# Optimization experiments

Measured on AMD Instinct MI355X. Metric: run time of the kernel, lower is better.

Reference implementation:

```python
import jax, jax.numpy as jnp
import numpy as np

B, C_IN, H, W = 4, 128, 32, 128   # W must equal out_channels (fc_out acts on last dim)
C_OUT, NUM_HEADS = 128, 2
BN_EPS = 1e-5


def setup_inputs() -> dict:
    key = jax.random.key(0)
    ks = jax.random.split(key, 14)
    s = 0.05  # small init scale for weights
    d = {
        "x": jax.random.normal(ks[0], (B, C_IN, H, W), jnp.float32),
        "wq": jax.random.normal(ks[1], (C_OUT, C_IN), jnp.float32) * s,
        "bq": jax.random.normal(ks[2], (C_OUT,), jnp.float32) * s,
        "wk": jax.random.normal(ks[3], (C_OUT, C_IN), jnp.float32) * s,
        "bk": jax.random.normal(ks[4], (C_OUT,), jnp.float32) * s,
        "wv": jax.random.normal(ks[5], (C_OUT, C_IN), jnp.float32) * s,
        "bv": jax.random.normal(ks[6], (C_OUT,), jnp.float32) * s,
        "fc_w": jax.random.normal(ks[7], (C_OUT, C_OUT), jnp.float32) * s,
        "fc_b": jax.random.normal(ks[8], (C_OUT,), jnp.float32) * s,
        "bn_gamma": jnp.ones((C_OUT,), jnp.float32),
        "bn_beta": jnp.zeros((C_OUT,), jnp.float32),
        "bn_mean": jax.random.normal(ks[9], (C_OUT,), jnp.float32) * 0.1,
        "bn_var": jax.random.uniform(ks[10], (C_OUT,), jnp.float32, 0.5, 1.5),
        "prelu_a": jnp.full((1,), 0.25, jnp.float32),
    }
    return d


def reference(x, wq, bq, wk, bk, wv, bv, fc_w, fc_b,
              bn_gamma, bn_beta, bn_mean, bn_var, prelu_a):
    b, c_in, h, w = x.shape
    c_out = wq.shape[0]
    nh = NUM_HEADS
    dk = c_out // nh
    L = h * w
    xf = x.reshape(b, c_in, L)                                # (B, Cin, L)
    # 1x1 convs == per-token linear projections
    q = jnp.einsum('oi,bil->bol', wq, xf) + bq[:, None]       # (B, Cout, L)
    k = jnp.einsum('oi,bil->bol', wk, xf) + bk[:, None]
    v = jnp.einsum('oi,bil->bol', wv, xf) + bv[:, None]
    Q = q.reshape(b, nh, dk, L)                               # (B, h, d_k, L)
    K = k.reshape(b, nh, dk, L)
    V = v.reshape(b, nh, dk, L)
    # scaled dot-product attention over the L = H*W tokens
    scores = jnp.einsum('bhdl,bhdm->bhlm', Q, K) / jnp.sqrt(jnp.float32(dk))
    attn = jax.nn.softmax(scores, axis=-1)                    # (B, h, L, L)
    out = jnp.einsum('bhlm,bhdm->bhdl', attn, V)              # (B, h, d_k, L)
    out = out.reshape(b, c_out, h, w)                         # (B, Cout, H, W)
    # fc_out: torch Linear on the LAST dim (W == Cout)
    y = jnp.einsum('bchw,ow->bcho', out, fc_w) + fc_b         # (B, Cout, H, W)
    # BatchNorm2d (eval mode: running stats) over channel dim
    inv = jax.lax.rsqrt(bn_var + BN_EPS)
    y = (y - bn_mean[None, :, None, None]) * (inv * bn_gamma)[None, :, None, None] \
        + bn_beta[None, :, None, None]
    # PReLU (single shared slope); dropout is identity in eval
    y = jnp.where(y > 0, y, prelu_a[0] * y)
    return y
```

## Files before the change

kernel.cpp:

```cpp
#include <hip/hip_runtime.h>

typedef _Float16 f16x8 __attribute__((ext_vector_type(8)));
typedef _Float16 f16x4t __attribute__((ext_vector_type(4)));
typedef __fp16 h16x2 __attribute__((ext_vector_type(2)));
typedef float f32x4 __attribute__((ext_vector_type(4)));
typedef float f32x16 __attribute__((ext_vector_type(16)));
typedef unsigned int uint2v __attribute__((ext_vector_type(2)));

#define L_SZ 4096

__device__ __forceinline__ unsigned short f2h(float f) {
    _Float16 h = (_Float16)f;
    return __builtin_bit_cast(unsigned short, h);
}
__device__ __forceinline__ unsigned int pk2(float a, float b) {
    h16x2 p = __builtin_amdgcn_cvt_pkrtz(a, b);
    return __builtin_bit_cast(unsigned int, p);
}

#define SLOT(row, ci) ((((ci) * 64) + ((row) & 32) + (((row) & 31) ^ (ci))) * 8)

__global__ __launch_bounds__(256) void prep_kernel(
    const float* __restrict__ wq, const float* __restrict__ wk,
    const float* __restrict__ wv, const float* __restrict__ fcw,
    unsigned short* __restrict__ Wimg, unsigned short* __restrict__ Fimg)
{
    int e2 = blockIdx.x * 256 + threadIdx.x;
    if (e2 < 24576) {
        const float* src = (e2 < 8192) ? wq : (e2 < 16384 ? wk : wv);
        float2 v = *(const float2*)&src[(e2 * 2) & 16383];
        int e = e2 * 2;
        int o = e >> 7, ci = (e & 127) >> 3, j = e & 7;
        *(unsigned int*)&Wimg[o * 128 + ((ci ^ (o & 15)) * 8) + j] = pk2(v.x, v.y);
    } else {
        int fe = (e2 - 24576) * 2;
        float2 v = *(const float2*)&fcw[fe];
        int o = fe >> 7, ci = (fe & 127) >> 3, j = fe & 7;
        *(unsigned int*)&Fimg[o * 128 + ((ci ^ (o & 15)) * 8) + j] = pk2(v.x, v.y);
    }
}

__global__ __launch_bounds__(256, 1) void qkv_kernel(
    const float* __restrict__ x,
    const unsigned short* __restrict__ Wimg,
    const float* __restrict__ bq, const float* __restrict__ bk,
    const float* __restrict__ bv,
    unsigned short* __restrict__ Qp, unsigned short* __restrict__ Kp,
    unsigned short* __restrict__ Vp)
{
    int blk = blockIdx.x;
    int bidx = blk >> 6;
    int l0 = (blk & 63) * 64;
    int tid = threadIdx.x;
    int wave = tid >> 6, lane = tid & 63;
    int c = lane & 15, qd = lane >> 4;

    __shared__ __align__(16) unsigned short Ws[384 * 128];
    __shared__ __align__(16) unsigned short Sc[9216];

    #pragma unroll
    for (int t = 0; t < 24; ++t) {
        int i8 = (tid + t * 256) * 8;
        *(uint4*)&Ws[i8] = *(const uint4*)&Wimg[i8];
    }

    unsigned short* Xs = Sc;
    #pragma unroll
    for (int it = 0; it < 8; ++it) {
        int i  = (tid >> 4) + 16 * it;
        int l4 = (tid & 15) * 4;
        const float4 v = *(const float4*)&x[(bidx * 128 + i) * L_SZ + l0 + l4];
        float vv[4] = {v.x, v.y, v.z, v.w};
        int ci = i >> 3;
        #pragma unroll
        for (int u = 0; u < 4; ++u) {
            int l = l4 + u;
            Xs[l * 128 + ((ci ^ (l & 15)) * 8) + (i & 7)] = f2h(vv[u]);
        }
    }
    __syncthreads();

    f16x8 afrag[4];
    #pragma unroll
    for (int kc = 0; kc < 4; ++kc) {
        int l = wave * 16 + c;
        int ci = kc * 4 + qd;
        afrag[kc] = *(const f16x8*)&Xs[l * 128 + ((ci ^ (l & 15)) * 8)];
    }
    __syncthreads();

    f32x4 acc[24];
    #pragma unroll
    for (int nt = 0; nt < 24; ++nt) acc[nt] = (f32x4){0.f, 0.f, 0.f, 0.f};

    #pragma unroll
    for (int kc = 0; kc < 4; ++kc) {
        #pragma unroll
        for (int nt = 0; nt < 24; ++nt) {
            int o = nt * 16 + c;
            f16x8 bfrag = *(const f16x8*)&Ws[o * 128 + (((kc * 4 + qd) ^ c) * 8)];
            acc[nt] = __builtin_amdgcn_mfma_f32_16x16x32_f16(afrag[kc], bfrag, acc[nt], 0, 0, 0);
        }
    }

    unsigned short* Vt = Sc;
    const float s_q = 0.18033688011f;
    #pragma unroll
    for (int nt = 0; nt < 24; ++nt) {
        int p = nt >> 3;
        int o = (nt & 7) * 16 + c;
        int h = o >> 6, d = o & 63;
        #pragma unroll
        for (int r = 0; r < 4; ++r) {
            int ll = wave * 16 + qd * 4 + r;
            int l = l0 + ll;
            float val = acc[nt][r];
            if (p == 0) {
                val = (val + bq[o]) * s_q;
                Qp[((bidx * 2 + h) * L_SZ + l) * 64 + d] = f2h(val);
            } else if (p == 1) {
                val += bk[o];
                Kp[((bidx * 2 + h) * L_SZ + l) * 64 + d] = f2h(val);
            } else {
                val += bv[o];
                Vt[o * 72 + ll] = f2h(val);
            }
        }
    }
    __syncthreads();
    #pragma unroll
    for (int t = 0; t < 2; ++t) {
        int u = tid + t * 256;
        int row = u >> 2;
        int lc = (u & 3) * 16;
        uint4 a0 = *(const uint4*)&Vt[row * 72 + lc];
        uint4 a1 = *(const uint4*)&Vt[row * 72 + lc + 8];
        *(uint4*)&Vp[(size_t)(bidx * 128 + row) * L_SZ + l0 + lc] = a0;
        *(uint4*)&Vp[(size_t)(bidx * 128 + row) * L_SZ + l0 + lc + 8] = a1;
    }
}

__global__ __launch_bounds__(256, 4) void attn_kernel(
    const unsigned short* __restrict__ Qp, const unsigned short* __restrict__ Kp,
    const unsigned short* __restrict__ Vp,
    unsigned short* __restrict__ Opart, float* __restrict__ Mpart, float* __restrict__ Lpart)
{
    int raw = blockIdx.x;
    int blk = (raw & 7) * 128 + (raw >> 3);
    int lt = blk & 31;
    int bh = (blk >> 5) & 7;
    int sp = blk >> 8;
    int l0 = lt * 128;
    int tid = threadIdx.x;
    int wave = tid >> 6, lane = tid & 63;
    int ln = lane & 31, hi = lane >> 5;
    int b = bh >> 1, h = bh & 1;

    __shared__ __align__(16) unsigned short Ks[2][4096];
    __shared__ __align__(16) unsigned short Vs[2][4096];

    const unsigned short* Qb = Qp + (size_t)bh * L_SZ * 64;
    const unsigned short* Kb = Kp + (size_t)bh * L_SZ * 64;
    const unsigned short* Vb = Vp + ((size_t)b * 128 + h * 64) * L_SZ;

    int lq = l0 + wave * 32 + ln;
    f16x8 qf[4];
    #pragma unroll
    for (int kc = 0; kc < 4; ++kc)
        qf[kc] = *(const f16x8*)&Qb[(size_t)lq * 64 + kc * 16 + hi * 8];

    float m_st = -1e30f, lsum = 0.f;
    f32x16 acc0 = {}, acc1 = {};

    int urow = tid >> 3, uci = tid & 7;
    int mglob = sp * 1024;

    uint4 kreg[2], vreg[2];
    #pragma unroll
    for (int j = 0; j < 2; ++j) {
        int row = urow + j * 32;
        kreg[j] = *(const uint4*)&Kb[(size_t)(mglob + row) * 64 + uci * 8];
        vreg[j] = *(const uint4*)&Vb[(size_t)row * L_SZ + mglob + uci * 8];
    }
    #pragma unroll
    for (int j = 0; j < 2; ++j) {
        int row = urow + j * 32;
        *(uint4*)&Ks[0][SLOT(row, uci)] = kreg[j];
        *(uint4*)&Vs[0][SLOT(row, uci)] = vreg[j];
    }

    for (int it = 0; it < 16; ++it) {
        int cur = it & 1;
        __syncthreads();
        if (it < 15) {
            int m0 = mglob + (it + 1) * 64;
            #pragma unroll
            for (int j = 0; j < 2; ++j) {
                int row = urow + j * 32;
                kreg[j] = *(const uint4*)&Kb[(size_t)(m0 + row) * 64 + uci * 8];
                vreg[j] = *(const uint4*)&Vb[(size_t)row * L_SZ + m0 + uci * 8];
            }
        }

        __builtin_amdgcn_s_setprio(1);
        f32x16 s0 = {}, s1 = {};
        #pragma unroll
        for (int kc = 0; kc < 4; ++kc) {
            int cd = kc * 2 + hi;
            f16x8 k0 = *(const f16x8*)&Ks[cur][SLOT(ln, cd)];
            f16x8 k1 = *(const f16x8*)&Ks[cur][SLOT(32 + ln, cd)];
            s0 = __builtin_amdgcn_mfma_f32_32x32x16_f16(k0, qf[kc], s0, 0, 0, 0);
            s1 = __builtin_amdgcn_mfma_f32_32x32x16_f16(k1, qf[kc], s1, 0, 0, 0);
        }

        float t[8];
        #pragma unroll
        for (int r = 0; r < 8; ++r)
            t[r] = fmaxf(fmaxf(s0[r], s0[r + 8]), fmaxf(s1[r], s1[r + 8]));
        t[0] = fmaxf(t[0], t[4]); t[1] = fmaxf(t[1], t[5]);
        t[2] = fmaxf(t[2], t[6]); t[3] = fmaxf(t[3], t[7]);
        float mx = fmaxf(fmaxf(t[0], t[1]), fmaxf(t[2], t[3]));
        mx = fmaxf(mx, __shfl_xor(mx, 32));

        if (!__all(mx <= m_st + 8.0f)) {
            float mnew = fmaxf(m_st, mx);
            float alpha = exp2f(m_st - mnew);
            m_st = mnew;
            lsum *= alpha;
            #pragma unroll
            for (int r = 0; r < 16; ++r) { acc0[r] *= alpha; acc1[r] *= alpha; }
        }
        float rsum = 0.f;
        #pragma unroll
        for (int r = 0; r < 16; ++r) { float p = exp2f(s0[r] - m_st); s0[r] = p; rsum += p; }
        #pragma unroll
        for (int r = 0; r < 16; ++r) { float p = exp2f(s1[r] - m_st); s1[r] = p; rsum += p; }
        lsum += rsum;

        #pragma unroll
        for (int kc = 0; kc < 4; ++kc) {
            unsigned int a0, a1, a2, a3;
            if (kc == 0) {
                a0 = pk2(s0[0], s0[1]);  a1 = pk2(s0[2], s0[3]);
                a2 = pk2(s0[4], s0[5]);  a3 = pk2(s0[6], s0[7]);
            } else if (kc == 1) {
                a0 = pk2(s0[8], s0[9]);  a1 = pk2(s0[10], s0[11]);
                a2 = pk2(s0[12], s0[13]); a3 = pk2(s0[14], s0[15]);
            } else if (kc == 2) {
                a0 = pk2(s1[0], s1[1]);  a1 = pk2(s1[2], s1[3]);
                a2 = pk2(s1[4], s1[5]);  a3 = pk2(s1[6], s1[7]);
            } else {
                a0 = pk2(s1[8], s1[9]);  a1 = pk2(s1[10], s1[11]);
                a2 = pk2(s1[12], s1[13]); a3 = pk2(s1[14], s1[15]);
            }
            uint2v r02 = __builtin_amdgcn_permlane32_swap(a0, a2, false, false);
            uint2v r13 = __builtin_amdgcn_permlane32_swap(a1, a3, false, false);
            uint4 pw; pw.x = r02[0]; pw.y = r13[0]; pw.z = r02[1]; pw.w = r13[1];
            f16x8 pf = __builtin_bit_cast(f16x8, pw);
            int cd = kc * 2 + hi;
            f16x8 v0 = *(const f16x8*)&Vs[cur][SLOT(ln, cd)];
            f16x8 v1 = *(const f16x8*)&Vs[cur][SLOT(32 + ln, cd)];
            acc0 = __builtin_amdgcn_mfma_f32_32x32x16_f16(v0, pf, acc0, 0, 0, 0);
            acc1 = __builtin_amdgcn_mfma_f32_32x32x16_f16(v1, pf, acc1, 0, 0, 0);
        }
        __builtin_amdgcn_s_setprio(0);

        if (it < 15) {
            #pragma unroll
            for (int j = 0; j < 2; ++j) {
                int row = urow + j * 32;
                *(uint4*)&Ks[cur ^ 1][SLOT(row, uci)] = kreg[j];
                *(uint4*)&Vs[cur ^ 1][SLOT(row, uci)] = vreg[j];
            }
        }
    }

    float l_tot = lsum + __shfl_xor(lsum, 32);
    unsigned short* Ow = Opart + (size_t)(sp * 8 + bh) * 64 * 4096;
    #pragma unroll
    for (int r = 0; r < 16; ++r) {
        int d0 = (r & 3) + 8 * (r >> 2) + 4 * hi;
        Ow[(size_t)d0 * 4096 + lq] = f2h(acc0[r]);
        Ow[(size_t)(32 + d0) * 4096 + lq] = f2h(acc1[r]);
    }
    if (hi == 0) {
        Mpart[(sp * 8 + bh) * 4096 + lq] = m_st;
        Lpart[(sp * 8 + bh) * 4096 + lq] = l_tot;
    }
}

__global__ __launch_bounds__(256, 1) void fc_kernel(
    const unsigned short* __restrict__ Opart, const float* __restrict__ Mp,
    const float* __restrict__ Lp, const unsigned short* __restrict__ Fimg,
    const float* __restrict__ fc_b, const float* __restrict__ bn_g,
    const float* __restrict__ bn_b, const float* __restrict__ bn_m,
    const float* __restrict__ bn_v, const float* __restrict__ prelu_a,
    float* __restrict__ out)
{
    int raw = blockIdx.x;
    int blk = (raw & 7) * 32 + (raw >> 3);
    int r0 = blk * 64;
    int tid = threadIdx.x;
    int c0 = (r0 >> 5) & 127;
    int bh = (r0 >> 12) * 2 + (c0 >> 6);

    int wave = tid >> 6, lane = tid & 63;
    int c = lane & 15, qd = lane >> 4;
    int rw = r0 + wave * 16;
    int row = rw + c;
    int ch = (row >> 5) & 127, hh = row & 31, d = ch & 63;

    __shared__ __align__(16) unsigned short Fw[128 * 128];
    __shared__ __align__(16) unsigned short SclU[4096 * 4];

    uint4 ovr[4][4];
    #pragma unroll
    for (int kc = 0; kc < 4; ++kc) {
        int w0 = kc * 32 + qd * 8;
        #pragma unroll
        for (int s = 0; s < 4; ++s)
            ovr[kc][s] = *(const uint4*)&Opart[(size_t)(s * 8 + bh) * 262144 + (size_t)d * 4096 + hh * 128 + w0];
    }

    #pragma unroll
    for (int t = 0; t < 16; ++t) {
        int l = tid + t * 256;
        float m0 = Mp[(0 * 8 + bh) * 4096 + l], m1 = Mp[(1 * 8 + bh) * 4096 + l];
        float m2 = Mp[(2 * 8 + bh) * 4096 + l], m3 = Mp[(3 * 8 + bh) * 4096 + l];
        float mx = fmaxf(fmaxf(m0, m1), fmaxf(m2, m3));
        float a0 = exp2f(m0 - mx), a1 = exp2f(m1 - mx);
        float a2 = exp2f(m2 - mx), a3 = exp2f(m3 - mx);
        float den = a0 * Lp[(0 * 8 + bh) * 4096 + l] + a1 * Lp[(1 * 8 + bh) * 4096 + l]
                  + a2 * Lp[(2 * 8 + bh) * 4096 + l] + a3 * Lp[(3 * 8 + bh) * 4096 + l];
        float inv = 1.0f / den;
        int hl = l >> 7, ww = l & 127;
        int slot = hl * 128 + ((ww + hl) & 127);
        uint2 sc;
        sc.x = pk2(a0 * inv, a1 * inv);
        sc.y = pk2(a2 * inv, a3 * inv);
        *(uint2*)&SclU[slot * 4] = sc;
    }
    #pragma unroll
    for (int t = 0; t < 8; ++t) {
        int i8 = (tid + t * 256) * 8;
        *(uint4*)&Fw[i8] = *(const uint4*)&Fimg[i8];
    }
    __syncthreads();

    f16x8 af[4];
    #pragma unroll
    for (int kc = 0; kc < 4; ++kc) {
        int w0 = kc * 32 + qd * 8;
        f16x8 ov0 = __builtin_bit_cast(f16x8, ovr[kc][0]);
        f16x8 ov1 = __builtin_bit_cast(f16x8, ovr[kc][1]);
        f16x8 ov2 = __builtin_bit_cast(f16x8, ovr[kc][2]);
        f16x8 ov3 = __builtin_bit_cast(f16x8, ovr[kc][3]);
        #pragma unroll
        for (int j = 0; j < 8; ++j) {
            int slot = hh * 128 + ((w0 + j + hh) & 127);
            f16x4t sc = *(const f16x4t*)&SclU[slot * 4];
            float v = (float)ov0[j] * (float)sc[0] + (float)ov1[j] * (float)sc[1]
                    + (float)ov2[j] * (float)sc[2] + (float)ov3[j] * (float)sc[3];
            af[kc][j] = (_Float16)v;
        }
    }

    f32x4 acc[8];
    #pragma unroll
    for (int nt = 0; nt < 8; ++nt) acc[nt] = (f32x4){0.f, 0.f, 0.f, 0.f};
    #pragma unroll
    for (int kc = 0; kc < 4; ++kc) {
        #pragma unroll
        for (int nt = 0; nt < 8; ++nt) {
            int o = nt * 16 + c;
            f16x8 bf = *(const f16x8*)&Fw[o * 128 + (((kc * 4 + qd) ^ c) * 8)];
            acc[nt] = __builtin_amdgcn_mfma_f32_16x16x32_f16(af[kc], bf, acc[nt], 0, 0, 0);
        }
    }

    float pa = prelu_a[0];
    #pragma unroll
    for (int r = 0; r < 4; ++r) {
        int orow = rw + qd * 4 + r;
        int chn = (orow >> 5) & 127;
        float g  = bn_g[chn] * rsqrtf(bn_v[chn] + 1e-5f);
        float mn = bn_m[chn], bt = bn_b[chn];
        #pragma unroll
        for (int nt = 0; nt < 8; ++nt) {
            int o = nt * 16 + c;
            float y = (acc[nt][r] + fc_b[o] - mn) * g + bt;
            y = y > 0.f ? y : pa * y;
            out[(size_t)orow * 128 + o] = y;
        }
    }
}

extern "C" void kernel_launch(void* const* d_in, const int* in_sizes, int n_in,
                              void* d_out, int out_size, void* d_ws, size_t ws_size,
                              hipStream_t stream) {
    const float* x     = (const float*)d_in[0];
    const float* wq    = (const float*)d_in[1];
    const float* bq    = (const float*)d_in[2];
    const float* wk    = (const float*)d_in[3];
    const float* bk    = (const float*)d_in[4];
    const float* wv    = (const float*)d_in[5];
    const float* bv    = (const float*)d_in[6];
    const float* fcw_f = (const float*)d_in[7];
    const float* fcb   = (const float*)d_in[8];
    const float* bn_g  = (const float*)d_in[9];
    const float* bn_b  = (const float*)d_in[10];
    const float* bn_m  = (const float*)d_in[11];
    const float* bn_v  = (const float*)d_in[12];
    const float* pa    = (const float*)d_in[13];
    float* out = (float*)d_out;

    unsigned short* Qp  = (unsigned short*)d_ws;
    unsigned short* Kp  = Qp + 8 * L_SZ * 64;
    unsigned short* Vp  = Kp + 8 * L_SZ * 64;
    unsigned short* Opart = Vp + 8 * L_SZ * 64;
    float* Mpart = (float*)(Opart + 4 * 8 * 64 * L_SZ);
    float* Lpart = Mpart + 4 * 8 * L_SZ;
    unsigned short* Wimg = (unsigned short*)(Lpart + 4 * 8 * L_SZ);
    unsigned short* Fimg = Wimg + 384 * 128;

    hipLaunchKernelGGL(prep_kernel, dim3(128),  dim3(256), 0, stream,
                       wq, wk, wv, fcw_f, Wimg, Fimg);
    hipLaunchKernelGGL(qkv_kernel,  dim3(256),  dim3(256), 0, stream,
                       x, Wimg, bq, bk, bv, Qp, Kp, Vp);
    hipLaunchKernelGGL(attn_kernel, dim3(1024), dim3(256), 0, stream,
                       Qp, Kp, Vp, Opart, Mpart, Lpart);
    hipLaunchKernelGGL(fc_kernel,   dim3(256),  dim3(256), 0, stream,
                       Opart, Mpart, Lpart, Fimg, fcb, bn_g, bn_b, bn_m, bn_v, pa, out);
}
```

Baseline: 172.7 us.

## Split QKV and FC kernels across more blocks and tune attention softmax inner loop

The QKV projection now launches one block per (tile, projection) triple with a 128x128 weight slice, which cuts shared memory and registers so more blocks fit per CU. The FC kernel halves its rows per block, splits output columns across waves and hoists the BN parameters since each block now covers one channel. The attention loop switches to pointer increments, partial unrolling, a restructured max reduction, split exp-sum accumulators and hardware exp2/rcp intrinsics. Together these aim to raise occupancy and instruction-level parallelism. The cost is that the x tile is reloaded three times, plus extra block launches.

```diff
diff --git a/kernel.cpp b/kernel.cpp
--- a/kernel.cpp
+++ b/kernel.cpp
@@ -16,6 +16,20 @@
 __device__ __forceinline__ unsigned int pk2(float a, float b) {
     h16x2 p = __builtin_amdgcn_cvt_pkrtz(a, b);
     return __builtin_bit_cast(unsigned int, p);
+}
+__device__ __forceinline__ float fexp2(float x) {
+#if __has_builtin(__builtin_amdgcn_exp2f)
+    return __builtin_amdgcn_exp2f(x);
+#else
+    return exp2f(x);
+#endif
+}
+__device__ __forceinline__ float frcp(float x) {
+#if __has_builtin(__builtin_amdgcn_rcpf)
+    return __builtin_amdgcn_rcpf(x);
+#else
+    return 1.0f / x;
+#endif
 }
 
 #define SLOT(row, ci) ((((ci) * 64) + ((row) & 32) + (((row) & 31) ^ (ci))) * 8)
@@ -40,7 +54,7 @@
     }
 }
 
-__global__ __launch_bounds__(256, 1) void qkv_kernel(
+__global__ __launch_bounds__(256, 3) void qkv_kernel(
     const float* __restrict__ x,
     const unsigned short* __restrict__ Wimg,
     const float* __restrict__ bq, const float* __restrict__ bk,
@@ -48,20 +62,24 @@
     unsigned short* __restrict__ Qp, unsigned short* __restrict__ Kp,
     unsigned short* __restrict__ Vp)
 {
-    int blk = blockIdx.x;
-    int bidx = blk >> 6;
-    int l0 = (blk & 63) * 64;
+    int raw = blockIdx.x;
+    int v = (raw & 7) * 96 + (raw >> 3);
+    int tile = v / 3;
+    int p = v - tile * 3;
+    int bidx = tile >> 6;
+    int l0 = (tile & 63) * 64;
     int tid = threadIdx.x;
     int wave = tid >> 6, lane = tid & 63;
     int c = lane & 15, qd = lane >> 4;
 
-    __shared__ __align__(16) unsigned short Ws[384 * 128];
+    __shared__ __align__(16) unsigned short Ws[128 * 128];
     __shared__ __align__(16) unsigned short Sc[9216];
 
-    #pragma unroll
-    for (int t = 0; t < 24; ++t) {
+    const unsigned short* wsrc = Wimg + p * 16384;
+    #pragma unroll
+    for (int t = 0; t < 8; ++t) {
         int i8 = (tid + t * 256) * 8;
-        *(uint4*)&Ws[i8] = *(const uint4*)&Wimg[i8];
+        *(uint4*)&Ws[i8] = *(const uint4*)&wsrc[i8];
     }
 
     unsigned short* Xs = Sc;
@@ -69,8 +87,8 @@
     for (int it = 0; it < 8; ++it) {
         int i  = (tid >> 4) + 16 * it;
         int l4 = (tid & 15) * 4;
-        const float4 v = *(const float4*)&x[(bidx * 128 + i) * L_SZ + l0 + l4];
-        float vv[4] = {v.x, v.y, v.z, v.w};
+        const float4 vx = *(const float4*)&x[(bidx * 128 + i) * L_SZ + l0 + l4];
+        float vv[4] = {vx.x, vx.y, vx.z, vx.w};
         int ci = i >> 3;
         #pragma unroll
         for (int u = 0; u < 4; ++u) {
@@ -89,54 +107,65 @@
     }
     __syncthreads();
 
-    f32x4 acc[24];
-    #pragma unroll
-    for (int nt = 0; nt < 24; ++nt) acc[nt] = (f32x4){0.f, 0.f, 0.f, 0.f};
+    f32x4 acc[8];
+    #pragma unroll
+    for (int nt = 0; nt < 8; ++nt) acc[nt] = (f32x4){0.f, 0.f, 0.f, 0.f};
 
     #pragma unroll
     for (int kc = 0; kc < 4; ++kc) {
         #pragma unroll
-        for (int nt = 0; nt < 24; ++nt) {
+        for (int nt = 0; nt < 8; ++nt) {
             int o = nt * 16 + c;
             f16x8 bfrag = *(const f16x8*)&Ws[o * 128 + (((kc * 4 + qd) ^ c) * 8)];
             acc[nt] = __builtin_amdgcn_mfma_f32_16x16x32_f16(afrag[kc], bfrag, acc[nt], 0, 0, 0);
         }
     }
 
-    unsigned short* Vt = Sc;
     const float s_q = 0.18033688011f;
-    #pragma unroll
-    for (int nt = 0; nt < 24; ++nt) {
-        int p = nt >> 3;
-        int o = (nt & 7) * 16 + c;
-        int h = o >> 6, d = o & 63;
-        #pragma unroll
-        for (int r = 0; r < 4; ++r) {
-            int ll = wave * 16 + qd * 4 + r;
-            int l = l0 + ll;
-            float val = acc[nt][r];
-            if (p == 0) {
-                val = (val + bq[o]) * s_q;
-                Qp[((bidx * 2 + h) * L_SZ + l) * 64 + d] = f2h(val);
-            } else if (p == 1) {
-                val += bk[o];
-                Kp[((bidx * 2 + h) * L_SZ + l) * 64 + d] = f2h(val);
-            } else {
-                val += bv[o];
-                Vt[o * 72 + ll] = f2h(val);
+    if (p == 0) {
+        #pragma unroll
+        for (int nt = 0; nt < 8; ++nt) {
+            int o = nt * 16 + c;
+            int h = o >> 6, d = o & 63;
+            #pragma unroll
+            for (int r = 0; r < 4; ++r) {
+                int l = l0 + wave * 16 + qd * 4 + r;
+                Qp[((bidx * 2 + h) * L_SZ + l) * 64 + d] = f2h((acc[nt][r] + bq[o]) * s_q);
             }
         }
-    }
-    __syncthreads();
-    #pragma unroll
-    for (int t = 0; t < 2; ++t) {
-        int u = tid + t * 256;
-        int row = u >> 2;
-        int lc = (u & 3) * 16;
-        uint4 a0 = *(const uint4*)&Vt[row * 72 + lc];
-        uint4 a1 = *(const uint4*)&Vt[row * 72 + lc + 8];
-        *(uint4*)&Vp[(size_t)(bidx * 128 + row) * L_SZ + l0 + lc] = a0;
-        *(uint4*)&Vp[(size_t)(bidx * 128 + row) * L_SZ + l0 + lc + 8] = a1;
+    } else if (p == 1) {
+        #pragma unroll
+        for (int nt = 0; nt < 8; ++nt) {
+            int o = nt * 16 + c;
+            int h = o >> 6, d = o & 63;
+            #pragma unroll
+            for (int r = 0; r < 4; ++r) {
+                int l = l0 + wave * 16 + qd * 4 + r;
+                Kp[((bidx * 2 + h) * L_SZ + l) * 64 + d] = f2h(acc[nt][r] + bk[o]);
+            }
+        }
+    } else {
+        unsigned short* Vt = Sc;
+        #pragma unroll
+        for (int nt = 0; nt < 8; ++nt) {
+            int o = nt * 16 + c;
+            #pragma unroll
+            for (int r = 0; r < 4; ++r) {
+                int ll = wave * 16 + qd * 4 + r;
+                Vt[o * 72 + ll] = f2h(acc[nt][r] + bv[o]);
+            }
+        }
+        __syncthreads();
+        #pragma unroll
+        for (int t = 0; t < 2; ++t) {
+            int u = tid + t * 256;
+            int row = u >> 2;
+            int lc = (u & 3) * 16;
+            uint4 a0 = *(const uint4*)&Vt[row * 72 + lc];
+            uint4 a1 = *(const uint4*)&Vt[row * 72 + lc + 8];
+            *(uint4*)&Vp[(size_t)(bidx * 128 + row) * L_SZ + l0 + lc] = a0;
+            *(uint4*)&Vp[(size_t)(bidx * 128 + row) * L_SZ + l0 + lc + 8] = a1;
+        }
     }
 }
 
@@ -175,13 +204,14 @@
     int urow = tid >> 3, uci = tid & 7;
     int mglob = sp * 1024;
 
+    const unsigned short* kptr = Kb + (size_t)(mglob + urow) * 64 + uci * 8;
+    const unsigned short* vptr = Vb + (size_t)urow * L_SZ + mglob + uci * 8;
+
     uint4 kreg[2], vreg[2];
-    #pragma unroll
-    for (int j = 0; j < 2; ++j) {
-        int row = urow + j * 32;
-        kreg[j] = *(const uint4*)&Kb[(size_t)(mglob + row) * 64 + uci * 8];
-        vreg[j] = *(const uint4*)&Vb[(size_t)row * L_SZ + mglob + uci * 8];
-    }
+    kreg[0] = *(const uint4*)(kptr);
+    kreg[1] = *(const uint4*)(kptr + 2048);
+    vreg[0] = *(const uint4*)(vptr);
+    vreg[1] = *(const uint4*)(vptr + 32 * L_SZ);
     #pragma unroll
     for (int j = 0; j < 2; ++j) {
         int row = urow + j * 32;
@@ -189,17 +219,16 @@
         *(uint4*)&Vs[0][SLOT(row, uci)] = vreg[j];
     }
 
+    #pragma unroll 2
     for (int it = 0; it < 16; ++it) {
         int cur = it & 1;
         __syncthreads();
         if (it < 15) {
-            int m0 = mglob + (it + 1) * 64;
-            #pragma unroll
-            for (int j = 0; j < 2; ++j) {
-                int row = urow + j * 32;
-                kreg[j] = *(const uint4*)&Kb[(size_t)(m0 + row) * 64 + uci * 8];
-                vreg[j] = *(const uint4*)&Vb[(size_t)row * L_SZ + m0 + uci * 8];
-            }
+            kptr += 4096; vptr += 64;
+            kreg[0] = *(const uint4*)(kptr);
+            kreg[1] = *(const uint4*)(kptr + 2048);
+            vreg[0] = *(const uint4*)(vptr);
+            vreg[1] = *(const uint4*)(vptr + 32 * L_SZ);
         }
 
         __builtin_amdgcn_s_setprio(1);
@@ -216,26 +245,39 @@
         float t[8];
         #pragma unroll
         for (int r = 0; r < 8; ++r)
-            t[r] = fmaxf(fmaxf(s0[r], s0[r + 8]), fmaxf(s1[r], s1[r + 8]));
-        t[0] = fmaxf(t[0], t[4]); t[1] = fmaxf(t[1], t[5]);
-        t[2] = fmaxf(t[2], t[6]); t[3] = fmaxf(t[3], t[7]);
-        float mx = fmaxf(fmaxf(t[0], t[1]), fmaxf(t[2], t[3]));
+            t[r] = fmaxf(fmaxf(s0[r], s0[r + 8]), s1[r]);
+        #pragma unroll
+        for (int r = 0; r < 4; ++r)
+            t[r] = fmaxf(fmaxf(t[r], t[r + 4]), s1[8 + r]);
+        float m01 = fmaxf(fmaxf(t[0], t[1]), s1[12]);
+        float m23 = fmaxf(fmaxf(t[2], t[3]), s1[13]);
+        float mx = fmaxf(fmaxf(m01, m23), fmaxf(s1[14], s1[15]));
         mx = fmaxf(mx, __shfl_xor(mx, 32));
 
         if (!__all(mx <= m_st + 8.0f)) {
             float mnew = fmaxf(m_st, mx);
-            float alpha = exp2f(m_st - mnew);
+            float alpha = fexp2(m_st - mnew);
             m_st = mnew;
             lsum *= alpha;
             #pragma unroll
             for (int r = 0; r < 16; ++r) { acc0[r] *= alpha; acc1[r] *= alpha; }
         }
-        float rsum = 0.f;
-        #pragma unroll
-        for (int r = 0; r < 16; ++r) { float p = exp2f(s0[r] - m_st); s0[r] = p; rsum += p; }
-        #pragma unroll
-        for (int r = 0; r < 16; ++r) { float p = exp2f(s1[r] - m_st); s1[r] = p; rsum += p; }
-        lsum += rsum;
+        float rs0 = 0.f, rs1 = 0.f, rs2 = 0.f, rs3 = 0.f;
+        #pragma unroll
+        for (int r = 0; r < 4; ++r) {
+            float p0 = fexp2(s0[r]      - m_st); s0[r]      = p0; rs0 += p0;
+            float p1 = fexp2(s0[r + 4]  - m_st); s0[r + 4]  = p1; rs1 += p1;
+            float p2 = fexp2(s0[r + 8]  - m_st); s0[r + 8]  = p2; rs2 += p2;
+            float p3 = fexp2(s0[r + 12] - m_st); s0[r + 12] = p3; rs3 += p3;
+        }
+        #pragma unroll
+        for (int r = 0; r < 4; ++r) {
+            float p0 = fexp2(s1[r]      - m_st); s1[r]      = p0; rs0 += p0;
+            float p1 = fexp2(s1[r + 4]  - m_st); s1[r + 4]  = p1; rs1 += p1;
+            float p2 = fexp2(s1[r + 8]  - m_st); s1[r + 8]  = p2; rs2 += p2;
+            float p3 = fexp2(s1[r + 12] - m_st); s1[r + 12] = p3; rs3 += p3;
+        }
+        lsum += (rs0 + rs1) + (rs2 + rs3);
 
         #pragma unroll
         for (int kc = 0; kc < 4; ++kc) {
@@ -289,7 +331,7 @@
     }
 }
 
-__global__ __launch_bounds__(256, 1) void fc_kernel(
+__global__ __launch_bounds__(256, 2) void fc_kernel(
     const unsigned short* __restrict__ Opart, const float* __restrict__ Mp,
     const float* __restrict__ Lp, const unsigned short* __restrict__ Fimg,
     const float* __restrict__ fc_b, const float* __restrict__ bn_g,
@@ -298,17 +340,18 @@
     float* __restrict__ out)
 {
     int raw = blockIdx.x;
-    int blk = (raw & 7) * 32 + (raw >> 3);
-    int r0 = blk * 64;
+    int blk = (raw & 7) * 64 + (raw >> 3);
+    int r0 = blk * 32;
     int tid = threadIdx.x;
-    int c0 = (r0 >> 5) & 127;
-    int bh = (r0 >> 12) * 2 + (c0 >> 6);
+    int c0 = blk & 127;
+    int bh = blk >> 6;
+    int d = c0 & 63;
 
     int wave = tid >> 6, lane = tid & 63;
     int c = lane & 15, qd = lane >> 4;
-    int rw = r0 + wave * 16;
-    int row = rw + c;
-    int ch = (row >> 5) & 127, hh = row & 31, d = ch & 63;
+    int rw = r0 + (wave >> 1) * 16;
+    int o0 = (wave & 1) * 64;
+    int hh = (rw + c) & 31;
 
     __shared__ __align__(16) unsigned short Fw[128 * 128];
     __shared__ __align__(16) unsigned short SclU[4096 * 4];
@@ -328,11 +371,11 @@
         float m0 = Mp[(0 * 8 + bh) * 4096 + l], m1 = Mp[(1 * 8 + bh) * 4096 + l];
         float m2 = Mp[(2 * 8 + bh) * 4096 + l], m3 = Mp[(3 * 8 + bh) * 4096 + l];
         float mx = fmaxf(fmaxf(m0, m1), fmaxf(m2, m3));
-        float a0 = exp2f(m0 - mx), a1 = exp2f(m1 - mx);
-        float a2 = exp2f(m2 - mx), a3 = exp2f(m3 - mx);
+        float a0 = fexp2(m0 - mx), a1 = fexp2(m1 - mx);
+        float a2 = fexp2(m2 - mx), a3 = fexp2(m3 - mx);
         float den = a0 * Lp[(0 * 8 + bh) * 4096 + l] + a1 * Lp[(1 * 8 + bh) * 4096 + l]
                   + a2 * Lp[(2 * 8 + bh) * 4096 + l] + a3 * Lp[(3 * 8 + bh) * 4096 + l];
-        float inv = 1.0f / den;
+        float inv = frcp(den);
         int hl = l >> 7, ww = l & 127;
         int slot = hl * 128 + ((ww + hl) & 127);
         uint2 sc;
@@ -365,29 +408,28 @@
         }
     }
 
-    f32x4 acc[8];
-    #pragma unroll
-    for (int nt = 0; nt < 8; ++nt) acc[nt] = (f32x4){0.f, 0.f, 0.f, 0.f};
+    f32x4 acc[4];
+    #pragma unroll
+    for (int nt = 0; nt < 4; ++nt) acc[nt] = (f32x4){0.f, 0.f, 0.f, 0.f};
     #pragma unroll
     for (int kc = 0; kc < 4; ++kc) {
         #pragma unroll
-        for (int nt = 0; nt < 8; ++nt) {
-            int o = nt * 16 + c;
+        for (int nt = 0; nt < 4; ++nt) {
+            int o = o0 + nt * 16 + c;
             f16x8 bf = *(const f16x8*)&Fw[o * 128 + (((kc * 4 + qd) ^ c) * 8)];
             acc[nt] = __builtin_amdgcn_mfma_f32_16x16x32_f16(af[kc], bf, acc[nt], 0, 0, 0);
         }
     }
 
     float pa = prelu_a[0];
+    float g  = bn_g[c0] * rsqrtf(bn_v[c0] + 1e-5f);
+    float mn = bn_m[c0], bt = bn_b[c0];
     #pragma unroll
     for (int r = 0; r < 4; ++r) {
         int orow = rw + qd * 4 + r;
-        int chn = (orow >> 5) & 127;
-        float g  = bn_g[chn] * rsqrtf(bn_v[chn] + 1e-5f);
-        float mn = bn_m[chn], bt = bn_b[chn];
-        #pragma unroll
-        for (int nt = 0; nt < 8; ++nt) {
-            int o = nt * 16 + c;
+        #pragma unroll
+        for (int nt = 0; nt < 4; ++nt) {
+            int o = o0 + nt * 16 + c;
             float y = (acc[nt][r] + fc_b[o] - mn) * g + bt;
             y = y > 0.f ? y : pa * y;
             out[(size_t)orow * 128 + o] = y;
@@ -425,10 +467,10 @@
 
     hipLaunchKernelGGL(prep_kernel, dim3(128),  dim3(256), 0, stream,
                        wq, wk, wv, fcw_f, Wimg, Fimg);
-    hipLaunchKernelGGL(qkv_kernel,  dim3(256),  dim3(256), 0, stream,
+    hipLaunchKernelGGL(qkv_kernel,  dim3(768),  dim3(256), 0, stream,
                        x, Wimg, bq, bk, bv, Qp, Kp, Vp);
     hipLaunchKernelGGL(attn_kernel, dim3(1024), dim3(256), 0, stream,
                        Qp, Kp, Vp, Opart, Mpart, Lpart);
-    hipLaunchKernelGGL(fc_kernel,   dim3(256),  dim3(256), 0, stream,
+    hipLaunchKernelGGL(fc_kernel,   dim3(512),  dim3(256), 0, stream,
                        Opart, Mpart, Lpart, Fimg, fcb, bn_g, bn_b, bn_m, bn_v, pa, out);
 }
```

Measured after the change: 183.1 us. 6.0% more time.
